# Kernel optimization log

Measured on AMD Instinct MI355X. Metric: run time of the kernel, lower is better.

The kernel has to match this reference:

```python
import jax, jax.numpy as jnp
import numpy as np

D_MODEL = 1024
N_HEAD = 16
D_K = D_MODEL // N_HEAD


def setup_inputs() -> dict:
    key = jax.random.key(0)
    ks = jax.random.split(key, 11)
    B, L = 8, 1024
    std = np.sqrt(2.0 / (D_MODEL + D_K)).astype(np.float32)
    inp = {
        "q": jax.random.normal(ks[0], (B, L, D_MODEL), jnp.float32),
        "k": jax.random.normal(ks[1], (B, L, D_MODEL), jnp.float32),
        "v": jax.random.normal(ks[2], (B, L, D_MODEL), jnp.float32),
        # Linear weights stored as [in, out] (transposed torch layout)
        "Wq": jax.random.normal(ks[3], (D_MODEL, D_MODEL), jnp.float32) * std,
        "bq": jnp.zeros((D_MODEL,), jnp.float32),
        "Wk": jax.random.normal(ks[4], (D_MODEL, D_MODEL), jnp.float32) * std,
        "bk": jnp.zeros((D_MODEL,), jnp.float32),
        "Wv": jax.random.normal(ks[5], (D_MODEL, D_MODEL), jnp.float32) * std,
        "bv": jnp.zeros((D_MODEL,), jnp.float32),
        "Wfc": jax.random.normal(ks[6], (D_MODEL, D_MODEL), jnp.float32) * np.sqrt(2.0 / (2 * D_MODEL)).astype(np.float32),
        "bfc": jnp.zeros((D_MODEL,), jnp.float32),
    }
    return inp


def reference(q, k, v, Wq, bq, Wk, bk, Wv, bv, Wfc, bfc):
    B, Lq, _ = q.shape
    Lk = k.shape[1]
    scale = 1.0 / np.sqrt(D_K).astype(np.float32)
    # projections -> [B, L, H, Dk]
    qh = (q @ Wq + bq).reshape(B, Lq, N_HEAD, D_K)
    kh = (k @ Wk + bk).reshape(B, Lk, N_HEAD, D_K)
    vh = (v @ Wv + bv).reshape(B, Lk, N_HEAD, D_K)
    # scores [B, H, Lq, Lk]
    attn = jnp.einsum("bqhd,bkhd->bhqk", qh, kh) * scale
    attn = jax.nn.softmax(attn, axis=-1)
    # dropout is identity in eval mode
    out = jnp.einsum("bhqk,bkhd->bqhd", attn, vh).reshape(B, Lq, N_HEAD * D_K)
    out = out @ Wfc + bfc
    # torch returns attn as [n_head*B, Lq, Lk] with head-major flattening
    attn_flat = jnp.transpose(attn, (1, 0, 2, 3)).reshape(N_HEAD * B, Lq, Lk)
    return out, attn_flat
```

## Files before the change

kernel.cpp:

```cpp
#include <hip/hip_runtime.h>
#include <stdint.h>

typedef __bf16 bf16;
typedef unsigned short u16;
typedef __bf16  bf16x8 __attribute__((ext_vector_type(8)));
typedef unsigned short u16x8 __attribute__((ext_vector_type(8)));
typedef float   f32x4  __attribute__((ext_vector_type(4)));

typedef __attribute__((address_space(1))) uint32_t gu32;
typedef __attribute__((address_space(3))) uint32_t su32;

__device__ __forceinline__ void async_cp16(const void* gp, void* sp) {
    __builtin_amdgcn_global_load_lds((const gu32*)gp, (su32*)sp, 16, 0, 0);
}

__global__ void detect_dtype(const u16* __restrict__ q, int* __restrict__ flag)
{
    __shared__ int cnt;
    if (threadIdx.x == 0) cnt = 0;
    __syncthreads();
    int c = 0;
    for (int i = threadIdx.x; i < 4096; i += 64) {
        const int e = (q[i] >> 7) & 0xFF;
        if (e >= 96 && e < 160) c++;
    }
    atomicAdd(&cnt, c);
    __syncthreads();
    if (threadIdx.x == 0) *flag = (cnt < 3500) ? 1 : 0;
}

__global__ __launch_bounds__(256) void convert_in(
    const void* __restrict__ src, bf16* __restrict__ dst, int n,
    const int* __restrict__ flagp)
{
    const bool srcF32 = (*flagp != 0);
    const int idx = blockIdx.x * 256 + threadIdx.x;
    if (idx * 8 >= n) return;
    bf16x8 v;
    if (srcF32) {
        const float4 a = ((const float4*)src)[idx * 2];
        const float4 b = ((const float4*)src)[idx * 2 + 1];
        v[0] = (bf16)a.x; v[1] = (bf16)a.y; v[2] = (bf16)a.z; v[3] = (bf16)a.w;
        v[4] = (bf16)b.x; v[5] = (bf16)b.y; v[6] = (bf16)b.z; v[7] = (bf16)b.w;
    } else {
        v = ((const bf16x8*)src)[idx];
    }
    ((bf16x8*)dst)[idx] = v;
}

__global__ __launch_bounds__(256) void gemm_bt128(
    const bf16* __restrict__ A, const bf16* __restrict__ BT,
    const bf16* __restrict__ bias, void* __restrict__ C,
    int M, int N, int K, const int* __restrict__ flagp)
{
    __shared__ alignas(16) bf16 As[128 * 32];
    __shared__ alignas(16) bf16 Bs[128 * 32];
    const bool outF32 = flagp && (*flagp != 0);
    const int tid  = threadIdx.x;
    const int lane = tid & 63, wave = tid >> 6;
    const int l16  = lane & 15, quad = lane >> 4;
    const int m0   = blockIdx.y * 128, n0 = blockIdx.x * 128;
    const int wm   = (wave >> 1) * 64, wn = (wave & 1) * 64;

    f32x4 acc[4][4];
#pragma unroll
    for (int i = 0; i < 4; i++)
#pragma unroll
        for (int j = 0; j < 4; j++) acc[i][j] = {0.f, 0.f, 0.f, 0.f};

    for (int k0 = 0; k0 < K; k0 += 32) {
#pragma unroll
        for (int i = 0; i < 2; i++) {
            const int c   = tid + 256 * i;
            const int row = c >> 2, cc = c & 3;
            async_cp16(A  + (size_t)(m0 + row) * K + k0 + cc * 8,
                       (char*)As + (size_t)(wave * 64 + 256 * i) * 16);
            async_cp16(BT + (size_t)(n0 + row) * K + k0 + cc * 8,
                       (char*)Bs + (size_t)(wave * 64 + 256 * i) * 16);
        }
        __syncthreads();
        bf16x8 af[4], bfr[4];
#pragma unroll
        for (int mi = 0; mi < 4; mi++)
            af[mi] = *(const bf16x8*)(As + (wm + mi * 16 + l16) * 32 + quad * 8);
#pragma unroll
        for (int ni = 0; ni < 4; ni++)
            bfr[ni] = *(const bf16x8*)(Bs + (wn + ni * 16 + l16) * 32 + quad * 8);
#pragma unroll
        for (int mi = 0; mi < 4; mi++)
#pragma unroll
            for (int ni = 0; ni < 4; ni++)
                acc[mi][ni] = __builtin_amdgcn_mfma_f32_16x16x32_bf16(
                    af[mi], bfr[ni], acc[mi][ni], 0, 0, 0);
        __syncthreads();
    }
#pragma unroll
    for (int ni = 0; ni < 4; ni++) {
        const int col = n0 + wn + ni * 16 + l16;
        const float bv = (float)bias[col];
#pragma unroll
        for (int mi = 0; mi < 4; mi++) {
#pragma unroll
            for (int r = 0; r < 4; r++) {
                const int row = m0 + wm + mi * 16 + quad * 4 + r;
                const float val = acc[mi][ni][r] + bv;
                if (outF32) ((float*)C)[(size_t)row * N + col] = val;
                else        ((bf16*)C)[(size_t)row * N + col] = (bf16)val;
            }
        }
    }
}

__global__ __launch_bounds__(256) void transpose_w(
    const void* __restrict__ src, u16* __restrict__ dst,
    const int* __restrict__ flagp)
{
    __shared__ alignas(16) u16 t[64][72];
    const bool srcF32 = (*flagp != 0);
    const int tid = threadIdx.x;
    const int r0 = blockIdx.y * 64, c0 = blockIdx.x * 64;
#pragma unroll
    for (int i = 0; i < 2; i++) {
        const int c = tid + 256 * i;
        const int r = c >> 3, ch = c & 7;
        u16x8 v;
        if (srcF32) {
            const float* sp = (const float*)src + (size_t)(r0 + r) * 1024 + c0 + ch * 8;
            const float4 a = *(const float4*)sp;
            const float4 b = *(const float4*)(sp + 4);
            bf16x8 bv;
            bv[0] = (bf16)a.x; bv[1] = (bf16)a.y; bv[2] = (bf16)a.z; bv[3] = (bf16)a.w;
            bv[4] = (bf16)b.x; bv[5] = (bf16)b.y; bv[6] = (bf16)b.z; bv[7] = (bf16)b.w;
            v = __builtin_bit_cast(u16x8, bv);
        } else {
            v = *(const u16x8*)((const u16*)src + (size_t)(r0 + r) * 1024 + c0 + ch * 8);
        }
        *(u16x8*)&t[r][ch * 8] = v;
    }
    __syncthreads();
#pragma unroll
    for (int i = 0; i < 2; i++) {
        const int c = tid + 256 * i;
        const int d = c >> 3, ch = c & 7;
        u16x8 v;
#pragma unroll
        for (int j = 0; j < 8; j++) v[j] = t[ch * 8 + j][d];
        *(u16x8*)(dst + (size_t)(c0 + d) * 1024 + r0 + ch * 8) = v;
    }
}

__global__ __launch_bounds__(256) void transpose_v(
    const u16* __restrict__ Vp, u16* __restrict__ Vt)
{
    __shared__ alignas(16) u16 t[64][72];
    const int tid = threadIdx.x;
    const int l0 = blockIdx.x * 64, h = blockIdx.y, b = blockIdx.z;
    const u16* src = Vp + (size_t)(b * 1024 + l0) * 1024 + h * 64;
#pragma unroll
    for (int i = 0; i < 2; i++) {
        const int c = tid + 256 * i;
        const int l = c >> 3, ch = c & 7;
        *(u16x8*)&t[l][ch * 8] = *(const u16x8*)(src + (size_t)l * 1024 + ch * 8);
    }
    __syncthreads();
    u16* dst = Vt + ((size_t)(b * 16 + h) * 64) * 1024 + l0;
#pragma unroll
    for (int i = 0; i < 2; i++) {
        const int c = tid + 256 * i;
        const int d = c >> 3, ch = c & 7;
        u16x8 v;
#pragma unroll
        for (int j = 0; j < 8; j++) v[j] = t[ch * 8 + j][d];
        *(u16x8*)(dst + (size_t)d * 1024 + ch * 8) = v;
    }
}

__global__ __launch_bounds__(256) void attn_scores(
    const bf16* __restrict__ Q, const bf16* __restrict__ Kp,
    void* __restrict__ Pout, const int* __restrict__ flagp)
{
    __shared__ float sc[16 * 1024];
    const bool outF32 = (*flagp != 0);
    const int tid  = threadIdx.x;
    const int lane = tid & 63, wave = tid >> 6;
    const int l16  = lane & 15, quad = lane >> 4;
    const int q0 = blockIdx.x * 16, h = blockIdx.y, b = blockIdx.z;
    const bf16* Qb = Q  + (size_t)(b * 1024 + q0) * 1024 + h * 64;
    const bf16* Kb = Kp + (size_t)b * 1024 * 1024 + h * 64;
    const bf16x8 a0 = *(const bf16x8*)(Qb + (size_t)l16 * 1024 + quad * 8);
    const bf16x8 a1 = *(const bf16x8*)(Qb + (size_t)l16 * 1024 + quad * 8 + 32);
#pragma unroll 4
    for (int t = 0; t < 16; ++t) {
        const int n0 = wave * 256 + t * 16;
        const bf16* kp = Kb + (size_t)(n0 + l16) * 1024 + quad * 8;
        const bf16x8 b0 = *(const bf16x8*)kp;
        const bf16x8 b1 = *(const bf16x8*)(kp + 32);
        f32x4 acc = {0.f, 0.f, 0.f, 0.f};
        acc = __builtin_amdgcn_mfma_f32_16x16x32_bf16(a0, b0, acc, 0, 0, 0);
        acc = __builtin_amdgcn_mfma_f32_16x16x32_bf16(a1, b1, acc, 0, 0, 0);
#pragma unroll
        for (int r = 0; r < 4; r++)
            sc[(quad * 4 + r) * 1024 + n0 + l16] = acc[r] * 0.125f;
    }
    __syncthreads();
    const int r = tid >> 4, g = tid & 15;
    float* row = sc + r * 1024;
    float m = -3.0e38f;
#pragma unroll
    for (int j = 0; j < 8; j++) {
        const float4 v0 = *(const float4*)(row + g * 8 + j * 128);
        const float4 v1 = *(const float4*)(row + g * 8 + j * 128 + 4);
        m = fmaxf(m, fmaxf(fmaxf(v0.x, v0.y), fmaxf(v0.z, v0.w)));
        m = fmaxf(m, fmaxf(fmaxf(v1.x, v1.y), fmaxf(v1.z, v1.w)));
    }
#pragma unroll
    for (int o = 8; o >= 1; o >>= 1) m = fmaxf(m, __shfl_xor(m, o, 16));
    float s = 0.f;
#pragma unroll
    for (int j = 0; j < 8; j++) {
        float4 v0 = *(float4*)(row + g * 8 + j * 128);
        float4 v1 = *(float4*)(row + g * 8 + j * 128 + 4);
        v0.x = __expf(v0.x - m); v0.y = __expf(v0.y - m);
        v0.z = __expf(v0.z - m); v0.w = __expf(v0.w - m);
        v1.x = __expf(v1.x - m); v1.y = __expf(v1.y - m);
        v1.z = __expf(v1.z - m); v1.w = __expf(v1.w - m);
        s += v0.x + v0.y + v0.z + v0.w + v1.x + v1.y + v1.z + v1.w;
        *(float4*)(row + g * 8 + j * 128) = v0;
        *(float4*)(row + g * 8 + j * 128 + 4) = v1;
    }
#pragma unroll
    for (int o = 8; o >= 1; o >>= 1) s += __shfl_xor(s, o, 16);
    const float inv = 1.f / s;
    const size_t rowbase = (size_t)((h * 8 + b) * 1024 + q0 + r) * 1024;
    if (outF32) {
        float* outp = (float*)Pout + 8388608 + rowbase;
#pragma unroll
        for (int j = 0; j < 8; j++) {
            float4 v0 = *(const float4*)(row + g * 8 + j * 128);
            float4 v1 = *(const float4*)(row + g * 8 + j * 128 + 4);
            v0.x *= inv; v0.y *= inv; v0.z *= inv; v0.w *= inv;
            v1.x *= inv; v1.y *= inv; v1.z *= inv; v1.w *= inv;
            *(float4*)(outp + g * 8 + j * 128) = v0;
            *(float4*)(outp + g * 8 + j * 128 + 4) = v1;
        }
    } else {
        bf16* outp = (bf16*)Pout + 8388608 + rowbase;
#pragma unroll
        for (int j = 0; j < 8; j++) {
            const float4 v0 = *(const float4*)(row + g * 8 + j * 128);
            const float4 v1 = *(const float4*)(row + g * 8 + j * 128 + 4);
            bf16x8 ov;
            ov[0] = (bf16)(v0.x * inv); ov[1] = (bf16)(v0.y * inv);
            ov[2] = (bf16)(v0.z * inv); ov[3] = (bf16)(v0.w * inv);
            ov[4] = (bf16)(v1.x * inv); ov[5] = (bf16)(v1.y * inv);
            ov[6] = (bf16)(v1.z * inv); ov[7] = (bf16)(v1.w * inv);
            *(bf16x8*)(outp + g * 8 + j * 128) = ov;
        }
    }
}

__global__ __launch_bounds__(256) void attn_pv(
    const void* __restrict__ Pv, const bf16* __restrict__ Vt,
    bf16* __restrict__ O, const int* __restrict__ flagp)
{
    __shared__ alignas(16) char PsRaw[16384];
    __shared__ alignas(16) bf16 Vs[64 * 32];
    const bool pF32 = (*flagp != 0);
    const int tid  = threadIdx.x;
    const int lane = tid & 63, wave = tid >> 6;
    const int l16  = lane & 15, quad = lane >> 4;
    const int m0 = blockIdx.x * 128, h = blockIdx.y, b = blockIdx.z;
    const size_t pbase = 8388608 + (size_t)((h * 8 + b) * 1024 + m0) * 1024;
    const bf16* Vb = Vt + ((size_t)(b * 16 + h) * 64) * 1024;
    f32x4 acc[2][4];
#pragma unroll
    for (int i = 0; i < 2; i++)
#pragma unroll
        for (int j = 0; j < 4; j++) acc[i][j] = {0.f, 0.f, 0.f, 0.f};

    for (int k0 = 0; k0 < 1024; k0 += 32) {
        if (pF32) {
            const float* Pf = (const float*)Pv + pbase;
#pragma unroll
            for (int i = 0; i < 4; i++) {
                const int c = tid + 256 * i;
                async_cp16(Pf + (size_t)(c >> 3) * 1024 + k0 + (c & 7) * 4,
                           PsRaw + (size_t)(wave * 64 + 256 * i) * 16);
            }
        } else {
            const bf16* Pb = (const bf16*)Pv + pbase;
#pragma unroll
            for (int i = 0; i < 2; i++) {
                const int c = tid + 256 * i;
                async_cp16(Pb + (size_t)(c >> 2) * 1024 + k0 + (c & 3) * 8,
                           PsRaw + (size_t)(wave * 64 + 256 * i) * 16);
            }
        }
        async_cp16(Vb + (size_t)(tid >> 2) * 1024 + k0 + (tid & 3) * 8,
                   (char*)Vs + (size_t)(wave * 64) * 16);
        __syncthreads();
        bf16x8 a[2], bb[4];
#pragma unroll
        for (int mi = 0; mi < 2; mi++) {
            const int prow = wave * 32 + mi * 16 + l16;
            if (pF32) {
                const float* pr = (const float*)PsRaw + prow * 32 + quad * 8;
#pragma unroll
                for (int j = 0; j < 8; j++) a[mi][j] = (bf16)pr[j];
            } else {
                a[mi] = *(const bf16x8*)((const bf16*)PsRaw + prow * 32 + quad * 8);
            }
        }
#pragma unroll
        for (int ni = 0; ni < 4; ni++)
            bb[ni] = *(const bf16x8*)(Vs + (ni * 16 + l16) * 32 + quad * 8);
#pragma unroll
        for (int mi = 0; mi < 2; mi++)
#pragma unroll
            for (int ni = 0; ni < 4; ni++)
                acc[mi][ni] = __builtin_amdgcn_mfma_f32_16x16x32_bf16(
                    a[mi], bb[ni], acc[mi][ni], 0, 0, 0);
        __syncthreads();
    }
    bf16* Ob = O + (size_t)b * 1024 * 1024 + h * 64;
#pragma unroll
    for (int mi = 0; mi < 2; mi++)
#pragma unroll
        for (int ni = 0; ni < 4; ni++)
#pragma unroll
            for (int r = 0; r < 4; r++) {
                const int row = m0 + wave * 32 + mi * 16 + quad * 4 + r;
                const int col = ni * 16 + l16;
                Ob[(size_t)row * 1024 + col] = (bf16)(acc[mi][ni][r]);
            }
}

extern "C" void kernel_launch(void* const* d_in, const int* in_sizes, int n_in,
                              void* d_out, int out_size, void* d_ws, size_t ws_size,
                              hipStream_t stream)
{
    const void* q   = d_in[0];
    const void* k   = d_in[1];
    const void* v   = d_in[2];
    const void* Wq  = d_in[3];
    const void* bq  = d_in[4];
    const void* Wk  = d_in[5];
    const void* bk  = d_in[6];
    const void* Wv  = d_in[7];
    const void* bv  = d_in[8];
    const void* Wfc = d_in[9];
    const void* bfc = d_in[10];

    const size_t M1 = 1024 * 1024;
    bf16* ws   = (bf16*)d_ws;
    bf16* WqT  = ws;
    bf16* WkT  = ws + 1 * M1;
    bf16* WvT  = ws + 2 * M1;
    bf16* WfcT = ws + 3 * M1;
    bf16* bB   = ws + 4 * M1;
    bf16* qb   = ws + 5 * M1;
    bf16* kb   = ws + 13 * M1;
    bf16* vb   = ws + 21 * M1;
    bf16* Qp   = ws + 29 * M1;
    bf16* Kp   = ws + 5 * M1;
    bf16* Vp   = ws + 13 * M1;
    bf16* Vt   = ws + 21 * M1;
    bf16* O    = ws + 13 * M1;
    int*  flag = (int*)(ws + 37 * M1);

    const dim3 tb(256);

    detect_dtype<<<1, 64, 0, stream>>>((const u16*)q, flag);

    convert_in<<<4096, tb, 0, stream>>>(q, qb, 8 * 1024 * 1024, flag);
    convert_in<<<4096, tb, 0, stream>>>(k, kb, 8 * 1024 * 1024, flag);
    convert_in<<<4096, tb, 0, stream>>>(v, vb, 8 * 1024 * 1024, flag);
    convert_in<<<1, tb, 0, stream>>>(bq,  bB + 0 * 2048, 1024, flag);
    convert_in<<<1, tb, 0, stream>>>(bk,  bB + 1 * 2048, 1024, flag);
    convert_in<<<1, tb, 0, stream>>>(bv,  bB + 2 * 2048, 1024, flag);
    convert_in<<<1, tb, 0, stream>>>(bfc, bB + 3 * 2048, 1024, flag);

    const dim3 tg(16, 16);
    transpose_w<<<tg, tb, 0, stream>>>(Wq,  (u16*)WqT,  flag);
    transpose_w<<<tg, tb, 0, stream>>>(Wk,  (u16*)WkT,  flag);
    transpose_w<<<tg, tb, 0, stream>>>(Wv,  (u16*)WvT,  flag);
    transpose_w<<<tg, tb, 0, stream>>>(Wfc, (u16*)WfcT, flag);

    const dim3 pg(8, 64);
    gemm_bt128<<<pg, tb, 0, stream>>>(qb, WqT, bB + 0 * 2048, Qp, 8192, 1024, 1024, nullptr);
    gemm_bt128<<<pg, tb, 0, stream>>>(kb, WkT, bB + 1 * 2048, Kp, 8192, 1024, 1024, nullptr);
    gemm_bt128<<<pg, tb, 0, stream>>>(vb, WvT, bB + 2 * 2048, Vp, 8192, 1024, 1024, nullptr);

    transpose_v<<<dim3(16, 16, 8), tb, 0, stream>>>((const u16*)Vp, (u16*)Vt);

    attn_scores<<<dim3(64, 16, 8), tb, 0, stream>>>(Qp, Kp, d_out, flag);

    attn_pv<<<dim3(8, 16, 8), tb, 0, stream>>>(d_out, Vt, O, flag);

    gemm_bt128<<<pg, tb, 0, stream>>>(O, WfcT, bB + 3 * 2048, d_out, 8192, 1024, 1024, flag);
}
```

Before: 1.196 ms.

## Fuse softmax-probability times V into the attention scores kernel

Merges the separate scores/softmax kernel and the P·V kernel into one. The normalized probabilities stay in registers, are written as bf16 into shared memory (padded row stride), and each wave then multiplies its 16-row P tile by a 16-column V slice directly. This avoids re-reading the large attention-probability matrix from global memory. The four bias-conversion launches are also collapsed into one kernel. The trade-off is that V is re-read per 16-query block with little reuse, and register pressure rises from holding 16 float4 per thread.

```diff
diff --git a/kernel.cpp b/kernel.cpp
--- a/kernel.cpp
+++ b/kernel.cpp
@@ -5,6 +5,7 @@
 typedef unsigned short u16;
 typedef __bf16  bf16x8 __attribute__((ext_vector_type(8)));
 typedef unsigned short u16x8 __attribute__((ext_vector_type(8)));
+typedef unsigned short u16x4 __attribute__((ext_vector_type(4)));
 typedef float   f32x4  __attribute__((ext_vector_type(4)));
 
 typedef __attribute__((address_space(1))) uint32_t gu32;
@@ -46,6 +47,26 @@
         v = ((const bf16x8*)src)[idx];
     }
     ((bf16x8*)dst)[idx] = v;
+}
+
+__global__ __launch_bounds__(256) void convert_bias4(
+    const void* __restrict__ b0, const void* __restrict__ b1,
+    const void* __restrict__ b2, const void* __restrict__ b3,
+    bf16* __restrict__ dst, const int* __restrict__ flagp)
+{
+    const bool srcF32 = (*flagp != 0);
+    const int tid = threadIdx.x;
+    const void* srcs[4] = {b0, b1, b2, b3};
+#pragma unroll
+    for (int t = 0; t < 4; t++) {
+        bf16* d = dst + t * 2048 + tid * 4;
+        if (srcF32) {
+            const float4 v = ((const float4*)srcs[t])[tid];
+            d[0] = (bf16)v.x; d[1] = (bf16)v.y; d[2] = (bf16)v.z; d[3] = (bf16)v.w;
+        } else {
+            *(u16x4*)d = *((const u16x4*)srcs[t] + tid);
+        }
+    }
 }
 
 __global__ __launch_bounds__(256) void gemm_bt128(
@@ -175,16 +196,18 @@
     }
 }
 
-__global__ __launch_bounds__(256) void attn_scores(
+__global__ __launch_bounds__(256) void attn_fused(
     const bf16* __restrict__ Q, const bf16* __restrict__ Kp,
+    const bf16* __restrict__ Vt, bf16* __restrict__ O,
     void* __restrict__ Pout, const int* __restrict__ flagp)
 {
-    __shared__ float sc[16 * 1024];
+    __shared__ alignas(16) float sc[16 * 1024];
     const bool outF32 = (*flagp != 0);
     const int tid  = threadIdx.x;
     const int lane = tid & 63, wave = tid >> 6;
     const int l16  = lane & 15, quad = lane >> 4;
     const int q0 = blockIdx.x * 16, h = blockIdx.y, b = blockIdx.z;
+
     const bf16* Qb = Q  + (size_t)(b * 1024 + q0) * 1024 + h * 64;
     const bf16* Kb = Kp + (size_t)b * 1024 * 1024 + h * 64;
     const bf16x8 a0 = *(const bf16x8*)(Qb + (size_t)l16 * 1024 + quad * 8);
@@ -203,136 +226,74 @@
             sc[(quad * 4 + r) * 1024 + n0 + l16] = acc[r] * 0.125f;
     }
     __syncthreads();
+
     const int r = tid >> 4, g = tid & 15;
-    float* row = sc + r * 1024;
+    const float* prow = sc + r * 1024 + g * 8;
+    float4 vv[16];
     float m = -3.0e38f;
 #pragma unroll
     for (int j = 0; j < 8; j++) {
-        const float4 v0 = *(const float4*)(row + g * 8 + j * 128);
-        const float4 v1 = *(const float4*)(row + g * 8 + j * 128 + 4);
-        m = fmaxf(m, fmaxf(fmaxf(v0.x, v0.y), fmaxf(v0.z, v0.w)));
-        m = fmaxf(m, fmaxf(fmaxf(v1.x, v1.y), fmaxf(v1.z, v1.w)));
+        vv[2 * j]     = *(const float4*)(prow + j * 128);
+        vv[2 * j + 1] = *(const float4*)(prow + j * 128 + 4);
+        m = fmaxf(m, fmaxf(fmaxf(vv[2 * j].x, vv[2 * j].y),
+                           fmaxf(vv[2 * j].z, vv[2 * j].w)));
+        m = fmaxf(m, fmaxf(fmaxf(vv[2 * j + 1].x, vv[2 * j + 1].y),
+                           fmaxf(vv[2 * j + 1].z, vv[2 * j + 1].w)));
     }
 #pragma unroll
     for (int o = 8; o >= 1; o >>= 1) m = fmaxf(m, __shfl_xor(m, o, 16));
     float s = 0.f;
 #pragma unroll
-    for (int j = 0; j < 8; j++) {
-        float4 v0 = *(float4*)(row + g * 8 + j * 128);
-        float4 v1 = *(float4*)(row + g * 8 + j * 128 + 4);
-        v0.x = __expf(v0.x - m); v0.y = __expf(v0.y - m);
-        v0.z = __expf(v0.z - m); v0.w = __expf(v0.w - m);
-        v1.x = __expf(v1.x - m); v1.y = __expf(v1.y - m);
-        v1.z = __expf(v1.z - m); v1.w = __expf(v1.w - m);
-        s += v0.x + v0.y + v0.z + v0.w + v1.x + v1.y + v1.z + v1.w;
-        *(float4*)(row + g * 8 + j * 128) = v0;
-        *(float4*)(row + g * 8 + j * 128 + 4) = v1;
+    for (int j = 0; j < 16; j++) {
+        vv[j].x = __expf(vv[j].x - m); vv[j].y = __expf(vv[j].y - m);
+        vv[j].z = __expf(vv[j].z - m); vv[j].w = __expf(vv[j].w - m);
+        s += vv[j].x + vv[j].y + vv[j].z + vv[j].w;
     }
 #pragma unroll
     for (int o = 8; o >= 1; o >>= 1) s += __shfl_xor(s, o, 16);
     const float inv = 1.f / s;
+#pragma unroll
+    for (int j = 0; j < 16; j++) {
+        vv[j].x *= inv; vv[j].y *= inv; vv[j].z *= inv; vv[j].w *= inv;
+    }
+    __syncthreads();
+
+    bf16* Pb = (bf16*)sc;
     const size_t rowbase = (size_t)((h * 8 + b) * 1024 + q0 + r) * 1024;
-    if (outF32) {
-        float* outp = (float*)Pout + 8388608 + rowbase;
-#pragma unroll
-        for (int j = 0; j < 8; j++) {
-            float4 v0 = *(const float4*)(row + g * 8 + j * 128);
-            float4 v1 = *(const float4*)(row + g * 8 + j * 128 + 4);
-            v0.x *= inv; v0.y *= inv; v0.z *= inv; v0.w *= inv;
-            v1.x *= inv; v1.y *= inv; v1.z *= inv; v1.w *= inv;
-            *(float4*)(outp + g * 8 + j * 128) = v0;
-            *(float4*)(outp + g * 8 + j * 128 + 4) = v1;
-        }
-    } else {
-        bf16* outp = (bf16*)Pout + 8388608 + rowbase;
-#pragma unroll
-        for (int j = 0; j < 8; j++) {
-            const float4 v0 = *(const float4*)(row + g * 8 + j * 128);
-            const float4 v1 = *(const float4*)(row + g * 8 + j * 128 + 4);
-            bf16x8 ov;
-            ov[0] = (bf16)(v0.x * inv); ov[1] = (bf16)(v0.y * inv);
-            ov[2] = (bf16)(v0.z * inv); ov[3] = (bf16)(v0.w * inv);
-            ov[4] = (bf16)(v1.x * inv); ov[5] = (bf16)(v1.y * inv);
-            ov[6] = (bf16)(v1.z * inv); ov[7] = (bf16)(v1.w * inv);
-            *(bf16x8*)(outp + g * 8 + j * 128) = ov;
-        }
-    }
-}
-
-__global__ __launch_bounds__(256) void attn_pv(
-    const void* __restrict__ Pv, const bf16* __restrict__ Vt,
-    bf16* __restrict__ O, const int* __restrict__ flagp)
-{
-    __shared__ alignas(16) char PsRaw[16384];
-    __shared__ alignas(16) bf16 Vs[64 * 32];
-    const bool pF32 = (*flagp != 0);
-    const int tid  = threadIdx.x;
-    const int lane = tid & 63, wave = tid >> 6;
-    const int l16  = lane & 15, quad = lane >> 4;
-    const int m0 = blockIdx.x * 128, h = blockIdx.y, b = blockIdx.z;
-    const size_t pbase = 8388608 + (size_t)((h * 8 + b) * 1024 + m0) * 1024;
-    const bf16* Vb = Vt + ((size_t)(b * 16 + h) * 64) * 1024;
-    f32x4 acc[2][4];
-#pragma unroll
-    for (int i = 0; i < 2; i++)
-#pragma unroll
-        for (int j = 0; j < 4; j++) acc[i][j] = {0.f, 0.f, 0.f, 0.f};
-
-    for (int k0 = 0; k0 < 1024; k0 += 32) {
-        if (pF32) {
-            const float* Pf = (const float*)Pv + pbase;
-#pragma unroll
-            for (int i = 0; i < 4; i++) {
-                const int c = tid + 256 * i;
-                async_cp16(Pf + (size_t)(c >> 3) * 1024 + k0 + (c & 7) * 4,
-                           PsRaw + (size_t)(wave * 64 + 256 * i) * 16);
-            }
+#pragma unroll
+    for (int j = 0; j < 8; j++) {
+        const float4 v0 = vv[2 * j], v1 = vv[2 * j + 1];
+        bf16x8 ov;
+        ov[0] = (bf16)v0.x; ov[1] = (bf16)v0.y; ov[2] = (bf16)v0.z; ov[3] = (bf16)v0.w;
+        ov[4] = (bf16)v1.x; ov[5] = (bf16)v1.y; ov[6] = (bf16)v1.z; ov[7] = (bf16)v1.w;
+        *(bf16x8*)(Pb + r * 1032 + g * 8 + j * 128) = ov;
+        if (outF32) {
+            float* outp = (float*)Pout + 8388608 + rowbase + g * 8 + j * 128;
+            *(float4*)outp = v0;
+            *(float4*)(outp + 4) = v1;
         } else {
-            const bf16* Pb = (const bf16*)Pv + pbase;
-#pragma unroll
-            for (int i = 0; i < 2; i++) {
-                const int c = tid + 256 * i;
-                async_cp16(Pb + (size_t)(c >> 2) * 1024 + k0 + (c & 3) * 8,
-                           PsRaw + (size_t)(wave * 64 + 256 * i) * 16);
-            }
-        }
-        async_cp16(Vb + (size_t)(tid >> 2) * 1024 + k0 + (tid & 3) * 8,
-                   (char*)Vs + (size_t)(wave * 64) * 16);
-        __syncthreads();
-        bf16x8 a[2], bb[4];
-#pragma unroll
-        for (int mi = 0; mi < 2; mi++) {
-            const int prow = wave * 32 + mi * 16 + l16;
-            if (pF32) {
-                const float* pr = (const float*)PsRaw + prow * 32 + quad * 8;
-#pragma unroll
-                for (int j = 0; j < 8; j++) a[mi][j] = (bf16)pr[j];
-            } else {
-                a[mi] = *(const bf16x8*)((const bf16*)PsRaw + prow * 32 + quad * 8);
-            }
-        }
-#pragma unroll
-        for (int ni = 0; ni < 4; ni++)
-            bb[ni] = *(const bf16x8*)(Vs + (ni * 16 + l16) * 32 + quad * 8);
-#pragma unroll
-        for (int mi = 0; mi < 2; mi++)
-#pragma unroll
-            for (int ni = 0; ni < 4; ni++)
-                acc[mi][ni] = __builtin_amdgcn_mfma_f32_16x16x32_bf16(
-                    a[mi], bb[ni], acc[mi][ni], 0, 0, 0);
-        __syncthreads();
-    }
-    bf16* Ob = O + (size_t)b * 1024 * 1024 + h * 64;
-#pragma unroll
-    for (int mi = 0; mi < 2; mi++)
-#pragma unroll
-        for (int ni = 0; ni < 4; ni++)
-#pragma unroll
-            for (int r = 0; r < 4; r++) {
-                const int row = m0 + wave * 32 + mi * 16 + quad * 4 + r;
-                const int col = ni * 16 + l16;
-                Ob[(size_t)row * 1024 + col] = (bf16)(acc[mi][ni][r]);
-            }
+            *(bf16x8*)((bf16*)Pout + 8388608 + rowbase + g * 8 + j * 128) = ov;
+        }
+    }
+    __syncthreads();
+
+    const bf16* Pfrag = Pb + l16 * 1032 + quad * 8;
+    const bf16* Vfrag = Vt + ((size_t)(b * 16 + h) * 64 + wave * 16 + l16) * 1024
+                           + quad * 8;
+    f32x4 acc0 = {0.f, 0.f, 0.f, 0.f}, acc1 = {0.f, 0.f, 0.f, 0.f};
+#pragma unroll 4
+    for (int k0 = 0; k0 < 1024; k0 += 64) {
+        const bf16x8 pa0 = *(const bf16x8*)(Pfrag + k0);
+        const bf16x8 vb0 = *(const bf16x8*)(Vfrag + k0);
+        const bf16x8 pa1 = *(const bf16x8*)(Pfrag + k0 + 32);
+        const bf16x8 vb1 = *(const bf16x8*)(Vfrag + k0 + 32);
+        acc0 = __builtin_amdgcn_mfma_f32_16x16x32_bf16(pa0, vb0, acc0, 0, 0, 0);
+        acc1 = __builtin_amdgcn_mfma_f32_16x16x32_bf16(pa1, vb1, acc1, 0, 0, 0);
+    }
+    bf16* Ob = O + (size_t)b * 1024 * 1024 + h * 64 + wave * 16 + l16;
+#pragma unroll
+    for (int rr = 0; rr < 4; rr++)
+        Ob[(size_t)(q0 + quad * 4 + rr) * 1024] = (bf16)(acc0[rr] + acc1[rr]);
 }
 
 extern "C" void kernel_launch(void* const* d_in, const int* in_sizes, int n_in,
@@ -375,10 +336,7 @@
     convert_in<<<4096, tb, 0, stream>>>(q, qb, 8 * 1024 * 1024, flag);
     convert_in<<<4096, tb, 0, stream>>>(k, kb, 8 * 1024 * 1024, flag);
     convert_in<<<4096, tb, 0, stream>>>(v, vb, 8 * 1024 * 1024, flag);
-    convert_in<<<1, tb, 0, stream>>>(bq,  bB + 0 * 2048, 1024, flag);
-    convert_in<<<1, tb, 0, stream>>>(bk,  bB + 1 * 2048, 1024, flag);
-    convert_in<<<1, tb, 0, stream>>>(bv,  bB + 2 * 2048, 1024, flag);
-    convert_in<<<1, tb, 0, stream>>>(bfc, bB + 3 * 2048, 1024, flag);
+    convert_bias4<<<1, tb, 0, stream>>>(bq, bk, bv, bfc, bB, flag);
 
     const dim3 tg(16, 16);
     transpose_w<<<tg, tb, 0, stream>>>(Wq,  (u16*)WqT,  flag);
@@ -393,9 +351,7 @@
 
     transpose_v<<<dim3(16, 16, 8), tb, 0, stream>>>((const u16*)Vp, (u16*)Vt);
 
-    attn_scores<<<dim3(64, 16, 8), tb, 0, stream>>>(Qp, Kp, d_out, flag);
-
-    attn_pv<<<dim3(8, 16, 8), tb, 0, stream>>>(d_out, Vt, O, flag);
+    attn_fused<<<dim3(64, 16, 8), tb, 0, stream>>>(Qp, Kp, Vt, O, d_out, flag);
 
     gemm_bt128<<<pg, tb, 0, stream>>>(O, WfcT, bB + 3 * 2048, d_out, 8192, 1024, 1024, flag);
 }
```

Result: faster. 1.060 ms (-11.4%).
